# Kernel optimization log

Measured on AMD Instinct MI355X. Metric: run time of the kernel, lower is better.

The kernel has to match this reference:

```python
import jax, jax.numpy as jnp
import numpy as np

N, E, IN_FEATS, H = 20000, 320000, 512, 64
EPS = 1e-5  # BatchNorm eps


def setup_inputs() -> dict:
    key = jax.random.key(0)
    ks = iter(jax.random.split(key, 64))
    rn = lambda *s: jax.random.normal(next(ks), s, dtype=jnp.float32)
    d = {}
    d["x"] = rn(N, IN_FEATS)
    d["edge_index"] = jax.random.randint(next(ks), (2, E), 0, N)
    d["Wm"] = rn(IN_FEATS, H) * 0.05; d["bm"] = rn(H) * 0.05
    d["Wc"] = rn(IN_FEATS, H) * 0.05; d["bc"] = rn(H) * 0.05
    d["Wg1"] = rn(H, 2 * H) * 0.05;     d["bg1"] = rn(2 * H) * 0.05
    d["Wg2"] = rn(2 * H, 2 * H) * 0.05; d["bg2"] = rn(2 * H) * 0.05
    d["Wg3"] = rn(2 * H, 4 * H) * 0.05; d["bg3"] = rn(4 * H) * 0.05
    for name, cin in (("e1", 8 * H), ("e2", 4 * H), ("e3", 4 * H)):
        d[name + "_gamma"] = 1.0 + rn(cin) * 0.1
        d[name + "_beta"] = rn(cin) * 0.1
        d[name + "_mean"] = rn(cin) * 0.1
        d[name + "_var"] = jax.random.uniform(next(ks), (cin,), dtype=jnp.float32) + 0.5
        d[name + "_W"] = rn(cin, 2 * H) * 0.05
    d["Wfc"] = rn(2 * H, 1) * 0.05; d["bfc"] = rn(1) * 0.05
    return d


def _gcn(x, W, b, src, dst, n):
    """PyG GCNConv: self-loops + symmetric normalization + sum aggregation."""
    h = x @ W  # [N, out]
    loop = jnp.arange(n)
    s = jnp.concatenate([src, loop])
    d = jnp.concatenate([dst, loop])
    deg = jax.ops.segment_sum(jnp.ones(s.shape[0], h.dtype), d, num_segments=n)
    dinv = jnp.where(deg > 0, jax.lax.rsqrt(deg), 0.0)
    msg = h[s] * (dinv[s] * dinv[d])[:, None]  # gather + normalize
    return jax.ops.segment_sum(msg, d, num_segments=n) + b


def _edge_conv(x, gamma, beta, mean, var, W, src, dst, n):
    """PyG EdgeConv with LinearPathPreact nn (BN->ReLU->Linear), max aggregation."""
    xi = x[dst]
    xj = x[src]
    feat = jnp.concatenate([xi, xj - xi], axis=-1)  # [E, 2*C]
    h = (feat - mean) * jax.lax.rsqrt(var + EPS) * gamma + beta  # BN (eval stats)
    h = jnp.maximum(h, 0.0) @ W  # ReLU -> Linear(bias=False)
    out = jax.ops.segment_max(h, dst, num_segments=n)
    return jnp.where(jnp.isfinite(out), out, 0.0)  # empty segments -> 0


def reference(x, edge_index, Wm, bm, Wc, bc, Wg1, bg1, Wg2, bg2, Wg3, bg3,
              e1_gamma, e1_beta, e1_mean, e1_var, e1_W,
              e2_gamma, e2_beta, e2_mean, e2_var, e2_W,
              e3_gamma, e3_beta, e3_mean, e3_var, e3_W,
              Wfc, bfc):
    n = x.shape[0]
    src, dst = edge_index[0], edge_index[1]
    x0_main = x @ Wm + bm
    x0 = x @ Wc + bc
    x0 = x0.at[0::4].set(x0_main[0::4])  # main-person rows use the main projection
    g = _gcn(x0, Wg1, bg1, src, dst, n)
    g = _gcn(g, Wg2, bg2, src, dst, n)
    g = _gcn(g, Wg3, bg3, src, dst, n)
    h = _edge_conv(g, e1_gamma, e1_beta, e1_mean, e1_var, e1_W, src, dst, n)
    h = _edge_conv(h, e2_gamma, e2_beta, e2_mean, e2_var, e2_W, src, dst, n)
    h = _edge_conv(h, e3_gamma, e3_beta, e3_mean, e3_var, e3_W, src, dst, n)
    return h @ Wfc + bfc  # [N, 1]
```

## Files before the change

kernel.cpp:

```cpp
#include <hip/hip_runtime.h>

#define DEVINL __device__ __forceinline__

constexpr int N_NODES  = 20000;
constexpr int N_EDGES  = 320000;
constexpr int IN_FEATS = 512;

static_assert(N_EDGES % 64 == 0, "edge tiling assumes E % 64 == 0");
static_assert(N_NODES % 16 == 0, "proj assumes N % 16 == 0");

typedef __attribute__((ext_vector_type(8))) short short8;
typedef __attribute__((ext_vector_type(4))) float f32x4;

DEVINL unsigned enc_f32(float v) {
  unsigned b = __float_as_uint(v);
  return (b & 0x80000000u) ? ~b : (b | 0x80000000u);
}
DEVINL float dec_f32(unsigned e) {
  unsigned b = (e & 0x80000000u) ? (e & 0x7FFFFFFFu) : ~e;
  return __uint_as_float(b);
}

DEVINL unsigned short bf16_rne(float f) {
  unsigned u = __float_as_uint(f);
  u += 0x7FFFu + ((u >> 16) & 1u);
  return (unsigned short)(u >> 16);
}
DEVINL void split_bf16(float v, unsigned short& h, unsigned short& l) {
  h = bf16_rne(v);
  float hf = __uint_as_float((unsigned)h << 16);
  l = bf16_rne(v - hf);
}

DEVINL void glds16(const unsigned short* g, unsigned short* l) {
  __builtin_amdgcn_global_load_lds(
      (const __attribute__((address_space(1))) unsigned int*)g,
      (__attribute__((address_space(3))) unsigned int*)l, 16, 0, 0);
}

__global__ void hist_kernel(const int* __restrict__ dst, int* __restrict__ cnt, int e) {
  int i = blockIdx.x * 256 + threadIdx.x;
  if (i < e) atomicAdd(&cnt[dst[i]], 1);
}
__global__ void dinv_kernel(const int* __restrict__ cnt, float* __restrict__ dinv,
                            float* __restrict__ dinv2, int n) {
  int i = blockIdx.x * 256 + threadIdx.x;
  if (i < n) {
    float s = rsqrtf((float)cnt[i] + 1.0f);
    dinv[i] = s;
    dinv2[i] = s * s;
  }
}
__global__ void __launch_bounds__(256)
scan_p1(const int* __restrict__ cnt, int* __restrict__ rp, int* __restrict__ bsum, int n) {
  __shared__ int buf[256];
  int i = blockIdx.x * 256 + threadIdx.x;
  int v = (i < n) ? cnt[i] : 0;
  buf[threadIdx.x] = v;
  __syncthreads();
  for (int off = 1; off < 256; off <<= 1) {
    int t = (threadIdx.x >= off) ? buf[threadIdx.x - off] : 0;
    __syncthreads();
    buf[threadIdx.x] += t;
    __syncthreads();
  }
  if (i < n) rp[i] = buf[threadIdx.x] - v;
  if (threadIdx.x == 255) bsum[blockIdx.x] = buf[255];
}
__global__ void __launch_bounds__(256)
scan_p2(int* __restrict__ bsum, int nb) {
  __shared__ int buf[256];
  int v = (threadIdx.x < nb) ? bsum[threadIdx.x] : 0;
  buf[threadIdx.x] = v;
  __syncthreads();
  for (int off = 1; off < 256; off <<= 1) {
    int t = (threadIdx.x >= off) ? buf[threadIdx.x - off] : 0;
    __syncthreads();
    buf[threadIdx.x] += t;
    __syncthreads();
  }
  if (threadIdx.x < nb) bsum[threadIdx.x] = buf[threadIdx.x] - v;
}
__global__ void __launch_bounds__(256)
scan_p3(int* __restrict__ rp, const int* __restrict__ bsum, int* __restrict__ cursor,
        int n, int e) {
  int i = blockIdx.x * 256 + threadIdx.x;
  if (i < n) {
    int v = rp[i] + bsum[blockIdx.x];
    rp[i] = v;
    cursor[i] = v;
  }
  if (i == 0) rp[n] = e;
}
__global__ void scatter_edges_kernel(const int* __restrict__ src, const int* __restrict__ dst,
                                     int* __restrict__ cursor, int* __restrict__ ssrc,
                                     int* __restrict__ sdst, int e) {
  int i = blockIdx.x * 256 + threadIdx.x;
  if (i < e) {
    int d = dst[i];
    int pos = atomicAdd(&cursor[d], 1);
    ssrc[pos] = src[i];
    sdst[pos] = d;
  }
}

__global__ void uvec1_kernel(const int* __restrict__ row_ptr, const int* __restrict__ ssrc,
                             const float* __restrict__ dinv, float* __restrict__ u1,
                             float* __restrict__ w1, int n) {
  int d = blockIdx.x * 256 + threadIdx.x;
  if (d >= n) return;
  float s = dinv[d];
  float acc = s;
  int e = row_ptr[d], end = row_ptr[d + 1];
  for (; e < end; ++e) acc += dinv[ssrc[e]];
  float u = s * acc;
  u1[d] = u;
  w1[d] = s * u;
}
__global__ void uvec2_kernel(const int* __restrict__ row_ptr, const int* __restrict__ ssrc,
                             const float* __restrict__ dinv, const float* __restrict__ w1,
                             float* __restrict__ u2, int n) {
  int d = blockIdx.x * 256 + threadIdx.x;
  if (d >= n) return;
  float acc = w1[d];
  int e = row_ptr[d], end = row_ptr[d + 1];
  for (; e < end; ++e) acc += w1[ssrc[e]];
  u2[d] = dinv[d] * acc;
}

__global__ void smallmm2(const float* __restrict__ A1, const float* __restrict__ B1,
                         float* __restrict__ C1, int m1, int k1, int n1,
                         const float* __restrict__ A2, const float* __restrict__ B2,
                         float* __restrict__ C2, int m2, int k2, int n2) {
  int i = blockIdx.x * 256 + threadIdx.x;
  int t1 = m1 * n1;
  if (i < t1) {
    int r = i / n1, c = i % n1;
    float acc = 0.f;
    for (int kk = 0; kk < k1; ++kk) acc = fmaf(A1[r * k1 + kk], B1[kk * n1 + c], acc);
    C1[i] = acc;
  } else {
    i -= t1;
    if (i < m2 * n2) {
      int r = i / n2, c = i % n2;
      float acc = 0.f;
      for (int kk = 0; kk < k2; ++kk) acc = fmaf(A2[r * k2 + kk], B2[kk * n2 + c], acc);
      C2[i] = acc;
    }
  }
}

DEVINL void bn1(const float* g, const float* b, const float* m, const float* v,
                float* sc, float* sh, int i) {
  float s = g[i] * rsqrtf(v[i] + 1e-5f);
  sc[i] = s;
  sh[i] = b[i] - m[i] * s;
}
__global__ void bn_prep_all(const float* g1, const float* b1, const float* m1, const float* v1,
                            float* sc1, float* sh1, const float* g2, const float* b2,
                            const float* m2, const float* v2, float* sc2, float* sh2,
                            const float* g3, const float* b3, const float* m3, const float* v3,
                            float* sc3, float* sh3) {
  int i = blockIdx.x * 256 + threadIdx.x;
  if (i < 512) bn1(g1, b1, m1, v1, sc1, sh1, i);
  else if (i < 768) bn1(g2, b2, m2, v2, sc2, sh2, i - 512);
  else if (i < 1024) bn1(g3, b3, m3, v3, sc3, sh3, i - 768);
}

DEVINL void wfrag1(const float* W, unsigned short* out, int e) {
  int k = e >> 7, c = e & 127;
  unsigned short h, l;
  split_bf16(W[e], h, l);
  int chunk = k >> 5, kq = (k >> 3) & 3, j = k & 7, ct = c >> 4, n = c & 15;
  int frag = (ct * 4 + kq) * 16 + n;
  size_t o = (size_t)chunk * 8192 + frag * 8 + j;
  out[o] = h;
  out[o + 4096] = l;
}
__global__ void wfrag_all(const float* __restrict__ e1W, const float* __restrict__ e2W,
                          const float* __restrict__ e3W, unsigned short* b1p,
                          unsigned short* b1q, unsigned short* b2p, unsigned short* b2q,
                          unsigned short* b3p, unsigned short* b3q) {
  int g = blockIdx.x * 256 + threadIdx.x;
  if (g < 32768) wfrag1(e1W, b1p, g);
  else if (g < 65536) wfrag1(e1W + 32768, b1q, g - 32768);
  else if (g < 81920) wfrag1(e2W, b2p, g - 65536);
  else if (g < 98304) wfrag1(e2W + 16384, b2q, g - 81920);
  else if (g < 114688) wfrag1(e3W, b3p, g - 98304);
  else wfrag1(e3W + 16384, b3q, g - 114688);
}

__global__ void combine_kernel(unsigned* __restrict__ Q, const float* __restrict__ P,
                               float* __restrict__ H, int n) {
  int i = blockIdx.x * 256 + threadIdx.x;
  if (i < n) {
    unsigned e = Q[i];
    H[i] = e ? (P[i] + dec_f32(e)) : 0.f;
    Q[i] = 0u;
  }
}

__global__ void __launch_bounds__(256)
proj_kernel(const float* __restrict__ X, const float* __restrict__ Wm,
            const float* __restrict__ bm, const float* __restrict__ Wc,
            const float* __restrict__ bc, const float* __restrict__ dinv,
            float* __restrict__ Y0) {
  __shared__ float xs[16][IN_FEATS];
  int tid = threadIdx.x;
  int rowBase = blockIdx.x * 16;
  for (int i = 0; i < 8; ++i) {
    int idx = i * 256 + tid;
    int r = idx >> 7, kq = idx & 127;
    *reinterpret_cast<float4*>(&xs[r][kq * 4]) =
        *reinterpret_cast<const float4*>(X + (size_t)(rowBase + r) * IN_FEATS + kq * 4);
  }
  __syncthreads();
  int r4 = tid >> 6;
  int j = tid & 63;
  const float* W = (r4 == 0) ? Wm : Wc;
  float a0 = 0.f, a1 = 0.f, a2 = 0.f, a3 = 0.f;
#pragma unroll 4
  for (int k = 0; k < IN_FEATS; ++k) {
    float w = W[k * 64 + j];
    a0 = fmaf(xs[r4][k], w, a0);
    a1 = fmaf(xs[r4 + 4][k], w, a1);
    a2 = fmaf(xs[r4 + 8][k], w, a2);
    a3 = fmaf(xs[r4 + 12][k], w, a3);
  }
  float b = (r4 == 0) ? bm[j] : bc[j];
  int r0 = rowBase + r4;
  Y0[(size_t)r0 * 64 + j] = (a0 + b) * dinv[r0];
  Y0[(size_t)(r0 + 4) * 64 + j] = (a1 + b) * dinv[r0 + 4];
  Y0[(size_t)(r0 + 8) * 64 + j] = (a2 + b) * dinv[r0 + 8];
  Y0[(size_t)(r0 + 12) * 64 + j] = (a3 + b) * dinv[r0 + 12];
}

template <int LOGF4>
__global__ void __launch_bounds__(256)
agg_kernel(const float* __restrict__ Y, const int* __restrict__ row_ptr,
           const int* __restrict__ ssrc, const float* __restrict__ mfac,
           float* __restrict__ Z, int n) {
  constexpr int F4 = 1 << LOGF4;
  int g = blockIdx.x * 256 + threadIdx.x;
  int d = g >> LOGF4, c4 = g & (F4 - 1);
  if (d >= n) return;
  const float4* Yp = (const float4*)Y;
  float4 a = Yp[(size_t)d * F4 + c4];
  float ax = a.x, ay = a.y, az = a.z, aw = a.w;
  int e = row_ptr[d], end = row_ptr[d + 1];
  for (; e + 7 < end; e += 8) {
    int s[8];
#pragma unroll
    for (int i = 0; i < 8; ++i) s[i] = ssrc[e + i];
    float4 v[8];
#pragma unroll
    for (int i = 0; i < 8; ++i) v[i] = Yp[(size_t)s[i] * F4 + c4];
#pragma unroll
    for (int i = 0; i < 8; ++i) {
      ax += v[i].x; ay += v[i].y; az += v[i].z; aw += v[i].w;
    }
  }
  for (; e < end; ++e) {
    float4 v = Yp[(size_t)ssrc[e] * F4 + c4];
    ax += v.x; ay += v.y; az += v.z; aw += v.w;
  }
  float s = mfac[d];
  ((float4*)Z)[(size_t)d * F4 + c4] = make_float4(ax * s, ay * s, az * s, aw * s);
}

__global__ void __launch_bounds__(256)
gemm_rank1_kernel(const float* __restrict__ X, const float* __restrict__ W,
                  const float* __restrict__ b3, const float* __restrict__ u1,
                  const float* __restrict__ u2, const float* __restrict__ c1,
                  const float* __restrict__ c2, float* __restrict__ H, int n) {
  constexpr int K = 64, F = 256;
  __shared__ float Xs[64][K + 1];
  __shared__ float Ws[K][65];
  int tid = threadIdx.x;
  int rowBase = blockIdx.x * 64;
  int colBase = blockIdx.y * 64;
  for (int idx = tid; idx < 64 * K; idx += 256) {
    int r = idx / K, k = idx % K;
    int row = rowBase + r;
    Xs[r][k] = (row < n) ? X[(size_t)row * K + k] : 0.f;
  }
  for (int idx = tid; idx < K * 64; idx += 256) {
    int k = idx >> 6, c = idx & 63;
    Ws[k][c] = W[(size_t)k * F + colBase + c];
  }
  __syncthreads();
  int tx = tid & 15, ty = tid >> 4;
  float acc[4][4] = {};
  for (int k = 0; k < K; ++k) {
    float a[4], b[4];
#pragma unroll
    for (int r = 0; r < 4; ++r) a[r] = Xs[ty * 4 + r][k];
#pragma unroll
    for (int c = 0; c < 4; ++c) b[c] = Ws[k][tx * 4 + c];
#pragma unroll
    for (int r = 0; r < 4; ++r)
#pragma unroll
      for (int c = 0; c < 4; ++c) acc[r][c] = fmaf(a[r], b[c], acc[r][c]);
  }
#pragma unroll
  for (int r = 0; r < 4; ++r) {
    int row = rowBase + ty * 4 + r;
    if (row < n) {
      float du2 = u2[row], du1 = u1[row];
#pragma unroll
      for (int c = 0; c < 4; ++c) {
        int col = colBase + tx * 4 + c;
        float v = acc[r][c] + du2 * c1[col] + du1 * c2[col] + b3[col];
        H[(size_t)row * F + col] = v;
      }
    }
  }
}

DEVINL void proc8(const float4& va, const float4& vb, const float4& sa, const float4& sb,
                  const float4& ha, const float4& hb, short8& hi, short8& lo) {
  float f[8] = {va.x, va.y, va.z, va.w, vb.x, vb.y, vb.z, vb.w};
  float s[8] = {sa.x, sa.y, sa.z, sa.w, sb.x, sb.y, sb.z, sb.w};
  float t[8] = {ha.x, ha.y, ha.z, ha.w, hb.x, hb.y, hb.z, hb.w};
#pragma unroll
  for (int j = 0; j < 8; ++j) {
    float v = fmaxf(fmaf(f[j], s[j], t[j]), 0.f);
    unsigned short hh, ll;
    split_bf16(v, hh, ll);
    hi[j] = (short)hh;
    lo[j] = (short)ll;
  }
}

template <int C>
__global__ void __launch_bounds__(256, 4)
ec_mfma_kernel(const float* __restrict__ X, const int* __restrict__ ssrc,
               const int* __restrict__ sdst,
               const float* __restrict__ scaleQ, const float* __restrict__ shiftQ,
               const unsigned short* __restrict__ BfragQ,
               const float* __restrict__ scaleP, const float* __restrict__ shiftP,
               const unsigned short* __restrict__ BfragP,
               unsigned* __restrict__ outU, float* __restrict__ outP,
               int nrows, int edge_blocks) {
  constexpr int NCH = C / 32;
  constexpr int NSTAGE = NCH / 2;
  __shared__ unsigned short Bmat[16384];
  __shared__ float ss[2 * C];
  __shared__ int de_s[64];
  const int tid = threadIdx.x, lane = tid & 63, wv = tid >> 6;
  const int q = lane >> 4, mn = lane & 15;
  const bool EDGE = (int)blockIdx.x < edge_blocks;
  const int base = (EDGE ? (int)blockIdx.x : (int)blockIdx.x - edge_blocks) * 64;
  const int koff = q * 8;
  const int lr = wv * 16 + mn;

  const float* scale = EDGE ? scaleQ : scaleP;
  const float* shift = EDGE ? shiftQ : shiftP;
  const unsigned short* Bfrag = EDGE ? BfragQ : BfragP;

  int id, is = 0;
  if (EDGE) {
    if (tid < 64) de_s[tid] = sdst[base + tid];
    is = ssrc[base + lr];
    id = sdst[base + lr];
  } else {
    id = min(base + lr, nrows - 1);
  }
  const float* pd = X + (size_t)id * C + koff;
  const float* ps = EDGE ? X + (size_t)is * C + koff : nullptr;

  f32x4 acc[8];
#pragma unroll
  for (int i = 0; i < 8; ++i) acc[i] = (f32x4)0.f;

  float4 A[2][4];
#define LOAD_A(cc, slot)                              \
  {                                                   \
    const int kk_ = (cc) * 32;                        \
    A[slot][0] = *(const float4*)(pd + kk_);          \
    A[slot][1] = *(const float4*)(pd + kk_ + 4);      \
    if (EDGE) {                                       \
      A[slot][2] = *(const float4*)(ps + kk_);        \
      A[slot][3] = *(const float4*)(ps + kk_ + 4);    \
    }                                                 \
  }

  LOAD_A(0, 0);
  {
    constexpr int NF4 = C / 4;
    if (tid < NF4)
      ((float4*)ss)[tid] = ((const float4*)scale)[tid];
    else if (tid < 2 * NF4)
      ((float4*)(ss + C))[tid - NF4] = ((const float4*)shift)[tid - NF4];
  }
  {
    const unsigned short* bs = Bfrag + lane * 8;
#pragma unroll
    for (int i = 0; i < 8; ++i) {
      int seg = wv * 8 + i;
      glds16(bs + seg * 512, Bmat + seg * 512);
    }
  }

#pragma unroll
  for (int s = 0; s < NSTAGE; ++s) {
    if (s > 0) {
      __syncthreads();
      const unsigned short* bs = Bfrag + (size_t)s * 16384 + lane * 8;
#pragma unroll
      for (int i = 0; i < 8; ++i) {
        int seg = wv * 8 + i;
        glds16(bs + seg * 512, Bmat + seg * 512);
      }
    }
    __syncthreads();
#pragma unroll
    for (int cc = 0; cc < 2; ++cc) {
      const int c = s * 2 + cc;
      const int kc = c * 32;
      if (c + 1 < NCH) LOAD_A(c + 1, (c + 1) & 1);
      float4 sca = *(const float4*)&ss[kc + koff];
      float4 scb = *(const float4*)&ss[kc + koff + 4];
      float4 sha = *(const float4*)&ss[C + kc + koff];
      float4 shb = *(const float4*)&ss[C + kc + koff + 4];
      const int sl = c & 1;
      float4 u0, u1;
      if (EDGE) {
        u0 = make_float4(A[sl][2].x - A[sl][0].x, A[sl][2].y - A[sl][0].y,
                         A[sl][2].z - A[sl][0].z, A[sl][2].w - A[sl][0].w);
        u1 = make_float4(A[sl][3].x - A[sl][1].x, A[sl][3].y - A[sl][1].y,
                         A[sl][3].z - A[sl][1].z, A[sl][3].w - A[sl][1].w);
      } else {
        u0 = A[sl][0];
        u1 = A[sl][1];
      }
      short8 ah, al;
      proc8(u0, u1, sca, scb, sha, shb, ah, al);
      const unsigned short* Bc = Bmat + cc * 8192;
#pragma unroll
      for (int ct = 0; ct < 8; ++ct) {
        int fi = ct * 64 + lane;
        short8 bh = *(const short8*)(Bc + fi * 8);
        short8 bl = *(const short8*)(Bc + 4096 + fi * 8);
        acc[ct] = __builtin_amdgcn_mfma_f32_16x16x32_bf16(ah, bh, acc[ct], 0, 0, 0);
        acc[ct] = __builtin_amdgcn_mfma_f32_16x16x32_bf16(ah, bl, acc[ct], 0, 0, 0);
        acc[ct] = __builtin_amdgcn_mfma_f32_16x16x32_bf16(al, bh, acc[ct], 0, 0, 0);
      }
    }
  }
#undef LOAD_A

  if (EDGE) {
    int e0 = wv * 16 + q * 4;
#pragma unroll
    for (int ct = 0; ct < 8; ++ct) {
      int f = ct * 16 + mn;
      int prev = de_s[e0];
      float mv = acc[ct][0];
#pragma unroll
      for (int r = 1; r < 4; ++r) {
        int d = de_s[e0 + r];
        float v = acc[ct][r];
        if (d == prev) {
          mv = fmaxf(mv, v);
        } else {
          atomicMax(&outU[(size_t)prev * 128 + f], enc_f32(mv));
          prev = d;
          mv = v;
        }
      }
      atomicMax(&outU[(size_t)prev * 128 + f], enc_f32(mv));
    }
  } else {
    int r0 = base + wv * 16 + q * 4;
#pragma unroll
    for (int ct = 0; ct < 8; ++ct) {
      int f = ct * 16 + mn;
#pragma unroll
      for (int r = 0; r < 4; ++r) {
        int row = r0 + r;
        if (row < nrows) outP[(size_t)row * 128 + f] = acc[ct][r];
      }
    }
  }
}

__global__ void __launch_bounds__(256)
fc_kernel(const unsigned* __restrict__ Q, const float* __restrict__ P,
          const float* __restrict__ Wfc, const float* __restrict__ bfc,
          float* __restrict__ out, int n) {
  int g = blockIdx.x * 256 + threadIdx.x;
  int node = g >> 6, lane = g & 63;
  if (node >= n) return;
  size_t b = (size_t)node * 128;
  unsigned q0 = Q[b + lane], q1 = Q[b + 64 + lane];
  float h0 = q0 ? (P[b + lane] + dec_f32(q0)) : 0.f;
  float h1 = q1 ? (P[b + 64 + lane] + dec_f32(q1)) : 0.f;
  float v = fmaf(h0, Wfc[lane], h1 * Wfc[64 + lane]);
#pragma unroll
  for (int off = 32; off > 0; off >>= 1) v += __shfl_down(v, off);
  if (lane == 0) out[node] = v + bfc[0];
}

extern "C" void kernel_launch(void* const* d_in, const int* in_sizes, int n_in,
                              void* d_out, int out_size, void* d_ws, size_t ws_size,
                              hipStream_t stream) {
  const float* x   = (const float*)d_in[0];
  const int*   ei  = (const int*)d_in[1];
  const float* Wm  = (const float*)d_in[2];
  const float* bm  = (const float*)d_in[3];
  const float* Wc  = (const float*)d_in[4];
  const float* bc  = (const float*)d_in[5];
  const float* Wg1 = (const float*)d_in[6];
  const float* bg1 = (const float*)d_in[7];
  const float* Wg2 = (const float*)d_in[8];
  const float* bg2 = (const float*)d_in[9];
  const float* Wg3 = (const float*)d_in[10];
  const float* bg3 = (const float*)d_in[11];
  const float* e1g = (const float*)d_in[12];
  const float* e1b = (const float*)d_in[13];
  const float* e1m = (const float*)d_in[14];
  const float* e1v = (const float*)d_in[15];
  const float* e1W = (const float*)d_in[16];
  const float* e2g = (const float*)d_in[17];
  const float* e2b = (const float*)d_in[18];
  const float* e2m = (const float*)d_in[19];
  const float* e2v = (const float*)d_in[20];
  const float* e2W = (const float*)d_in[21];
  const float* e3g = (const float*)d_in[22];
  const float* e3b = (const float*)d_in[23];
  const float* e3m = (const float*)d_in[24];
  const float* e3v = (const float*)d_in[25];
  const float* e3W = (const float*)d_in[26];
  const float* Wfc = (const float*)d_in[27];
  const float* bfc = (const float*)d_in[28];

  const int* src = ei;
  const int* dst = ei + N_EDGES;

  float* ws    = (float*)d_ws;
  float* dinv  = ws;
  float* dinv2 = dinv + N_NODES;
  float* u1    = dinv2 + N_NODES;
  float* w1    = u1 + N_NODES;
  float* u2    = w1 + N_NODES;
  float* y0    = u2 + N_NODES;
  float* za    = y0 + (size_t)N_NODES * 64;
  float* zb    = za + (size_t)N_NODES * 64;
  float* PQ    = zb + (size_t)N_NODES * 64;
  float* G     = PQ + (size_t)N_NODES * 256;
  float* sc1   = G + (size_t)N_NODES * 256;
  float* sh1   = sc1 + 512;
  float* sc2   = sh1 + 512;
  float* sh2   = sc2 + 256;
  float* sc3   = sh2 + 256;
  float* sh3   = sc3 + 256;
  unsigned short* bf1p = (unsigned short*)(sh3 + 256);
  unsigned short* bf1q = bf1p + 65536;
  unsigned short* bf2p = bf1q + 65536;
  unsigned short* bf2q = bf2p + 32768;
  unsigned short* bf3p = bf2q + 32768;
  unsigned short* bf3q = bf3p + 32768;
  float* W23   = (float*)(bf3q + 32768);
  float* W123  = W23 + 32768;
  float* c1    = W123 + 16384;
  float* c2    = c1 + 256;
  int* cnt     = (int*)(c2 + 256);
  int* row_ptr = cnt + N_NODES;
  int* cursor  = row_ptr + N_NODES + 1;
  int* bsum    = cursor + N_NODES;
  int* ssrc    = bsum + 256;
  int* sdst    = ssrc + N_EDGES;

  float*    Pbuf = PQ;
  unsigned* Qbuf = (unsigned*)(PQ + (size_t)N_NODES * 128);

  hipMemsetAsync(cnt, 0, N_NODES * sizeof(int), stream);
  hist_kernel<<<N_EDGES / 256, 256, 0, stream>>>(dst, cnt, N_EDGES);
  dinv_kernel<<<79, 256, 0, stream>>>(cnt, dinv, dinv2, N_NODES);
  scan_p1<<<79, 256, 0, stream>>>(cnt, row_ptr, bsum, N_NODES);
  scan_p2<<<1, 256, 0, stream>>>(bsum, 79);
  scan_p3<<<79, 256, 0, stream>>>(row_ptr, bsum, cursor, N_NODES, N_EDGES);
  scatter_edges_kernel<<<N_EDGES / 256, 256, 0, stream>>>(src, dst, cursor, ssrc, sdst,
                                                          N_EDGES);

  smallmm2<<<129, 256, 0, stream>>>(Wg2, Wg3, W23, 128, 128, 256,
                                    bg2, Wg3, c2, 1, 128, 256);
  smallmm2<<<65, 256, 0, stream>>>(Wg1, W23, W123, 64, 128, 256,
                                   bg1, W23, c1, 1, 128, 256);
  uvec1_kernel<<<79, 256, 0, stream>>>(row_ptr, ssrc, dinv, u1, w1, N_NODES);
  uvec2_kernel<<<79, 256, 0, stream>>>(row_ptr, ssrc, dinv, w1, u2, N_NODES);

  bn_prep_all<<<4, 256, 0, stream>>>(e1g, e1b, e1m, e1v, sc1, sh1, e2g, e2b, e2m, e2v, sc2,
                                     sh2, e3g, e3b, e3m, e3v, sc3, sh3);
  wfrag_all<<<512, 256, 0, stream>>>(e1W, e2W, e3W, bf1p, bf1q, bf2p, bf2q, bf3p, bf3q);

  proj_kernel<<<N_NODES / 16, 256, 0, stream>>>(x, Wm, bm, Wc, bc, dinv, y0);
  agg_kernel<4><<<N_NODES * 16 / 256, 256, 0, stream>>>(y0, row_ptr, ssrc, dinv2, za, N_NODES);
  agg_kernel<4><<<N_NODES * 16 / 256, 256, 0, stream>>>(za, row_ptr, ssrc, dinv2, zb, N_NODES);
  agg_kernel<4><<<N_NODES * 16 / 256, 256, 0, stream>>>(zb, row_ptr, ssrc, dinv, za, N_NODES);
  dim3 grid4(313, 4);
  gemm_rank1_kernel<<<grid4, 256, 0, stream>>>(za, W123, bg3, u1, u2, c1, c2, G, N_NODES);

  const int EDGE_BLOCKS = N_EDGES / 64;
  const int NODE_BLOCKS = (N_NODES + 63) / 64;
  const int EC_BLOCKS   = EDGE_BLOCKS + NODE_BLOCKS;
  const int NB_ELEM     = N_NODES * 128 / 256;

  float* H1 = G;
  float* H2 = G + (size_t)N_NODES * 128;

  hipMemsetAsync(Qbuf, 0, (size_t)N_NODES * 128 * 4, stream);
  ec_mfma_kernel<256><<<EC_BLOCKS, 256, 0, stream>>>(
      G, ssrc, sdst, sc1 + 256, sh1 + 256, bf1q, sc1, sh1, bf1p, Qbuf, Pbuf, N_NODES,
      EDGE_BLOCKS);
  combine_kernel<<<NB_ELEM, 256, 0, stream>>>(Qbuf, Pbuf, H1, N_NODES * 128);

  ec_mfma_kernel<128><<<EC_BLOCKS, 256, 0, stream>>>(
      H1, ssrc, sdst, sc2 + 128, sh2 + 128, bf2q, sc2, sh2, bf2p, Qbuf, Pbuf, N_NODES,
      EDGE_BLOCKS);
  combine_kernel<<<NB_ELEM, 256, 0, stream>>>(Qbuf, Pbuf, H2, N_NODES * 128);

  ec_mfma_kernel<128><<<EC_BLOCKS, 256, 0, stream>>>(
      H2, ssrc, sdst, sc3 + 128, sh3 + 128, bf3q, sc3, sh3, bf3p, Qbuf, Pbuf, N_NODES,
      EDGE_BLOCKS);
  fc_kernel<<<N_NODES * 64 / 256, 256, 0, stream>>>(Qbuf, Pbuf, Wfc, bfc, (float*)d_out,
                                                    N_NODES);
}
```

Baseline: 710.3 us.

## Fuse combine step into edge-conv loads and merge small setup kernels

The separate combine kernels that decoded the max-encoded Q and added P into dense H buffers are removed. The second and third edge-conv kernels now read Q and P directly and decode them on the fly for both the source and destination rows, using ping-pong P/Q buffers with a memset before each layer. The dinv computation is folded into scan_p1, and the BN-prep and weight-fragment kernels are merged into one launch. This saves two full elementwise passes and several launches, but doubles the gathered bytes per edge in layers 2 and 3 and lowers the occupancy bound to 3 blocks for the combine variant.

After: 742.0 us. +4.5%, slower.

```diff
diff --git a/kernel.cpp b/kernel.cpp
--- a/kernel.cpp
+++ b/kernel.cpp
@@ -20,6 +20,7 @@
   unsigned b = (e & 0x80000000u) ? (e & 0x7FFFFFFFu) : ~e;
   return __uint_as_float(b);
 }
+DEVINL float dech(unsigned q, float p) { return q ? (p + dec_f32(q)) : 0.f; }
 
 DEVINL unsigned short bf16_rne(float f) {
   unsigned u = __float_as_uint(f);
@@ -42,20 +43,17 @@
   int i = blockIdx.x * 256 + threadIdx.x;
   if (i < e) atomicAdd(&cnt[dst[i]], 1);
 }
-__global__ void dinv_kernel(const int* __restrict__ cnt, float* __restrict__ dinv,
-                            float* __restrict__ dinv2, int n) {
-  int i = blockIdx.x * 256 + threadIdx.x;
-  if (i < n) {
-    float s = rsqrtf((float)cnt[i] + 1.0f);
-    dinv[i] = s;
-    dinv2[i] = s * s;
-  }
-}
 __global__ void __launch_bounds__(256)
-scan_p1(const int* __restrict__ cnt, int* __restrict__ rp, int* __restrict__ bsum, int n) {
+scan_p1(const int* __restrict__ cnt, int* __restrict__ rp, int* __restrict__ bsum,
+        float* __restrict__ dinv, float* __restrict__ dinv2, int n) {
   __shared__ int buf[256];
   int i = blockIdx.x * 256 + threadIdx.x;
   int v = (i < n) ? cnt[i] : 0;
+  if (i < n) {
+    float s = rsqrtf((float)v + 1.0f);
+    dinv[i] = s;
+    dinv2[i] = s * s;
+  }
   buf[threadIdx.x] = v;
   __syncthreads();
   for (int off = 1; off < 256; off <<= 1) {
@@ -156,17 +154,6 @@
   sc[i] = s;
   sh[i] = b[i] - m[i] * s;
 }
-__global__ void bn_prep_all(const float* g1, const float* b1, const float* m1, const float* v1,
-                            float* sc1, float* sh1, const float* g2, const float* b2,
-                            const float* m2, const float* v2, float* sc2, float* sh2,
-                            const float* g3, const float* b3, const float* m3, const float* v3,
-                            float* sc3, float* sh3) {
-  int i = blockIdx.x * 256 + threadIdx.x;
-  if (i < 512) bn1(g1, b1, m1, v1, sc1, sh1, i);
-  else if (i < 768) bn1(g2, b2, m2, v2, sc2, sh2, i - 512);
-  else if (i < 1024) bn1(g3, b3, m3, v3, sc3, sh3, i - 768);
-}
-
 DEVINL void wfrag1(const float* W, unsigned short* out, int e) {
   int k = e >> 7, c = e & 127;
   unsigned short h, l;
@@ -177,26 +164,29 @@
   out[o] = h;
   out[o + 4096] = l;
 }
-__global__ void wfrag_all(const float* __restrict__ e1W, const float* __restrict__ e2W,
-                          const float* __restrict__ e3W, unsigned short* b1p,
-                          unsigned short* b1q, unsigned short* b2p, unsigned short* b2q,
-                          unsigned short* b3p, unsigned short* b3q) {
-  int g = blockIdx.x * 256 + threadIdx.x;
-  if (g < 32768) wfrag1(e1W, b1p, g);
-  else if (g < 65536) wfrag1(e1W + 32768, b1q, g - 32768);
-  else if (g < 81920) wfrag1(e2W, b2p, g - 65536);
-  else if (g < 98304) wfrag1(e2W + 16384, b2q, g - 81920);
-  else if (g < 114688) wfrag1(e3W, b3p, g - 98304);
-  else wfrag1(e3W + 16384, b3q, g - 114688);
-}
-
-__global__ void combine_kernel(unsigned* __restrict__ Q, const float* __restrict__ P,
-                               float* __restrict__ H, int n) {
-  int i = blockIdx.x * 256 + threadIdx.x;
-  if (i < n) {
-    unsigned e = Q[i];
-    H[i] = e ? (P[i] + dec_f32(e)) : 0.f;
-    Q[i] = 0u;
+__global__ void setup_kernel(const float* __restrict__ e1W, const float* __restrict__ e2W,
+                             const float* __restrict__ e3W, unsigned short* b1p,
+                             unsigned short* b1q, unsigned short* b2p, unsigned short* b2q,
+                             unsigned short* b3p, unsigned short* b3q,
+                             const float* g1, const float* b1, const float* m1,
+                             const float* v1, float* sc1, float* sh1, const float* g2,
+                             const float* b2, const float* m2, const float* v2, float* sc2,
+                             float* sh2, const float* g3, const float* b3, const float* m3,
+                             const float* v3, float* sc3, float* sh3) {
+  if (blockIdx.x < 512) {
+    int g = blockIdx.x * 256 + threadIdx.x;
+    if (g < 32768) wfrag1(e1W, b1p, g);
+    else if (g < 65536) wfrag1(e1W + 32768, b1q, g - 32768);
+    else if (g < 81920) wfrag1(e2W, b2p, g - 65536);
+    else if (g < 98304) wfrag1(e2W + 16384, b2q, g - 81920);
+    else if (g < 114688) wfrag1(e3W, b3p, g - 98304);
+    else wfrag1(e3W + 16384, b3q, g - 114688);
+  } else {
+    for (int i = threadIdx.x; i < 1024; i += 256) {
+      if (i < 512) bn1(g1, b1, m1, v1, sc1, sh1, i);
+      else if (i < 768) bn1(g2, b2, m2, v2, sc2, sh2, i - 512);
+      else bn1(g3, b3, m3, v3, sc3, sh3, i - 768);
+    }
   }
 }
 
@@ -331,10 +321,14 @@
     lo[j] = (short)ll;
   }
 }
-
-template <int C>
-__global__ void __launch_bounds__(256, 4)
-ec_mfma_kernel(const float* __restrict__ X, const int* __restrict__ ssrc,
+DEVINL float4 dec4(uint4 q, float4 p) {
+  return make_float4(dech(q.x, p.x), dech(q.y, p.y), dech(q.z, p.z), dech(q.w, p.w));
+}
+
+template <int C, bool COMBINE>
+__global__ void __launch_bounds__(256, COMBINE ? 3 : 4)
+ec_mfma_kernel(const float* __restrict__ X, const unsigned* __restrict__ Qin,
+               const float* __restrict__ Pin, const int* __restrict__ ssrc,
                const int* __restrict__ sdst,
                const float* __restrict__ scaleQ, const float* __restrict__ shiftQ,
                const unsigned short* __restrict__ BfragQ,
@@ -366,23 +360,54 @@
   } else {
     id = min(base + lr, nrows - 1);
   }
-  const float* pd = X + (size_t)id * C + koff;
-  const float* ps = EDGE ? X + (size_t)is * C + koff : nullptr;
 
   f32x4 acc[8];
 #pragma unroll
   for (int i = 0; i < 8; ++i) acc[i] = (f32x4)0.f;
 
+  const float* pd = nullptr;
+  const float* pvs = nullptr;
+  const unsigned* qd = nullptr;
+  const float* ppd = nullptr;
+  const unsigned* qs = nullptr;
+  const float* pps = nullptr;
+  if (COMBINE) {
+    qd = Qin + (size_t)id * C + koff;
+    ppd = Pin + (size_t)id * C + koff;
+    if (EDGE) {
+      qs = Qin + (size_t)is * C + koff;
+      pps = Pin + (size_t)is * C + koff;
+    }
+  } else {
+    pd = X + (size_t)id * C + koff;
+    if (EDGE) pvs = X + (size_t)is * C + koff;
+  }
+
   float4 A[2][4];
-#define LOAD_A(cc, slot)                              \
-  {                                                   \
-    const int kk_ = (cc) * 32;                        \
-    A[slot][0] = *(const float4*)(pd + kk_);          \
-    A[slot][1] = *(const float4*)(pd + kk_ + 4);      \
-    if (EDGE) {                                       \
-      A[slot][2] = *(const float4*)(ps + kk_);        \
-      A[slot][3] = *(const float4*)(ps + kk_ + 4);    \
-    }                                                 \
+  uint4 Aq[2][4];
+  float4 Ap[2][4];
+#define LOAD_A(cc, slot)                                        \
+  {                                                             \
+    const int kk_ = (cc) * 32;                                  \
+    if (COMBINE) {                                              \
+      Aq[slot][0] = *(const uint4*)(qd + kk_);                  \
+      Aq[slot][1] = *(const uint4*)(qd + kk_ + 4);              \
+      Ap[slot][0] = *(const float4*)(ppd + kk_);                \
+      Ap[slot][1] = *(const float4*)(ppd + kk_ + 4);            \
+      if (EDGE) {                                               \
+        Aq[slot][2] = *(const uint4*)(qs + kk_);                \
+        Aq[slot][3] = *(const uint4*)(qs + kk_ + 4);            \
+        Ap[slot][2] = *(const float4*)(pps + kk_);              \
+        Ap[slot][3] = *(const float4*)(pps + kk_ + 4);          \
+      }                                                         \
+    } else {                                                    \
+      A[slot][0] = *(const float4*)(pd + kk_);                  \
+      A[slot][1] = *(const float4*)(pd + kk_ + 4);              \
+      if (EDGE) {                                               \
+        A[slot][2] = *(const float4*)(pvs + kk_);               \
+        A[slot][3] = *(const float4*)(pvs + kk_ + 4);           \
+      }                                                         \
+    }                                                           \
   }
 
   LOAD_A(0, 0);
@@ -425,14 +450,28 @@
       float4 shb = *(const float4*)&ss[C + kc + koff + 4];
       const int sl = c & 1;
       float4 u0, u1;
-      if (EDGE) {
-        u0 = make_float4(A[sl][2].x - A[sl][0].x, A[sl][2].y - A[sl][0].y,
-                         A[sl][2].z - A[sl][0].z, A[sl][2].w - A[sl][0].w);
-        u1 = make_float4(A[sl][3].x - A[sl][1].x, A[sl][3].y - A[sl][1].y,
-                         A[sl][3].z - A[sl][1].z, A[sl][3].w - A[sl][1].w);
+      if (COMBINE) {
+        float4 hd0 = dec4(Aq[sl][0], Ap[sl][0]);
+        float4 hd1 = dec4(Aq[sl][1], Ap[sl][1]);
+        if (EDGE) {
+          float4 hs0 = dec4(Aq[sl][2], Ap[sl][2]);
+          float4 hs1 = dec4(Aq[sl][3], Ap[sl][3]);
+          u0 = make_float4(hs0.x - hd0.x, hs0.y - hd0.y, hs0.z - hd0.z, hs0.w - hd0.w);
+          u1 = make_float4(hs1.x - hd1.x, hs1.y - hd1.y, hs1.z - hd1.z, hs1.w - hd1.w);
+        } else {
+          u0 = hd0;
+          u1 = hd1;
+        }
       } else {
-        u0 = A[sl][0];
-        u1 = A[sl][1];
+        if (EDGE) {
+          u0 = make_float4(A[sl][2].x - A[sl][0].x, A[sl][2].y - A[sl][0].y,
+                           A[sl][2].z - A[sl][0].z, A[sl][2].w - A[sl][0].w);
+          u1 = make_float4(A[sl][3].x - A[sl][1].x, A[sl][3].y - A[sl][1].y,
+                           A[sl][3].z - A[sl][1].z, A[sl][3].w - A[sl][1].w);
+        } else {
+          u0 = A[sl][0];
+          u1 = A[sl][1];
+        }
       }
       short8 ah, al;
       proc8(u0, u1, sca, scb, sha, shb, ah, al);
@@ -493,9 +532,8 @@
   int node = g >> 6, lane = g & 63;
   if (node >= n) return;
   size_t b = (size_t)node * 128;
-  unsigned q0 = Q[b + lane], q1 = Q[b + 64 + lane];
-  float h0 = q0 ? (P[b + lane] + dec_f32(q0)) : 0.f;
-  float h1 = q1 ? (P[b + 64 + lane] + dec_f32(q1)) : 0.f;
+  float h0 = dech(Q[b + lane], P[b + lane]);
+  float h1 = dech(Q[b + 64 + lane], P[b + 64 + lane]);
   float v = fmaf(h0, Wfc[lane], h1 * Wfc[64 + lane]);
 #pragma unroll
   for (int off = 32; off > 0; off >>= 1) v += __shfl_down(v, off);
@@ -572,13 +610,16 @@
   int* ssrc    = bsum + 256;
   int* sdst    = ssrc + N_EDGES;
 
-  float*    Pbuf = PQ;
-  unsigned* Qbuf = (unsigned*)(PQ + (size_t)N_NODES * 128);
+  float*    P1 = PQ;
+  unsigned* Q1 = (unsigned*)(PQ + (size_t)N_NODES * 128);
+  float*    P2 = G;
+  unsigned* Q2 = (unsigned*)(G + (size_t)N_NODES * 128);
+  float*    P3 = P1;
+  unsigned* Q3 = Q1;
 
   hipMemsetAsync(cnt, 0, N_NODES * sizeof(int), stream);
   hist_kernel<<<N_EDGES / 256, 256, 0, stream>>>(dst, cnt, N_EDGES);
-  dinv_kernel<<<79, 256, 0, stream>>>(cnt, dinv, dinv2, N_NODES);
-  scan_p1<<<79, 256, 0, stream>>>(cnt, row_ptr, bsum, N_NODES);
+  scan_p1<<<79, 256, 0, stream>>>(cnt, row_ptr, bsum, dinv, dinv2, N_NODES);
   scan_p2<<<1, 256, 0, stream>>>(bsum, 79);
   scan_p3<<<79, 256, 0, stream>>>(row_ptr, bsum, cursor, N_NODES, N_EDGES);
   scatter_edges_kernel<<<N_EDGES / 256, 256, 0, stream>>>(src, dst, cursor, ssrc, sdst,
@@ -591,9 +632,9 @@
   uvec1_kernel<<<79, 256, 0, stream>>>(row_ptr, ssrc, dinv, u1, w1, N_NODES);
   uvec2_kernel<<<79, 256, 0, stream>>>(row_ptr, ssrc, dinv, w1, u2, N_NODES);
 
-  bn_prep_all<<<4, 256, 0, stream>>>(e1g, e1b, e1m, e1v, sc1, sh1, e2g, e2b, e2m, e2v, sc2,
-                                     sh2, e3g, e3b, e3m, e3v, sc3, sh3);
-  wfrag_all<<<512, 256, 0, stream>>>(e1W, e2W, e3W, bf1p, bf1q, bf2p, bf2q, bf3p, bf3q);
+  setup_kernel<<<513, 256, 0, stream>>>(e1W, e2W, e3W, bf1p, bf1q, bf2p, bf2q, bf3p, bf3q,
+                                        e1g, e1b, e1m, e1v, sc1, sh1, e2g, e2b, e2m, e2v,
+                                        sc2, sh2, e3g, e3b, e3m, e3v, sc3, sh3);
 
   proj_kernel<<<N_NODES / 16, 256, 0, stream>>>(x, Wm, bm, Wc, bc, dinv, y0);
   agg_kernel<4><<<N_NODES * 16 / 256, 256, 0, stream>>>(y0, row_ptr, ssrc, dinv2, za, N_NODES);
@@ -605,25 +646,22 @@
   const int EDGE_BLOCKS = N_EDGES / 64;
   const int NODE_BLOCKS = (N_NODES + 63) / 64;
   const int EC_BLOCKS   = EDGE_BLOCKS + NODE_BLOCKS;
-  const int NB_ELEM     = N_NODES * 128 / 256;
-
-  float* H1 = G;
-  float* H2 = G + (size_t)N_NODES * 128;
-
-  hipMemsetAsync(Qbuf, 0, (size_t)N_NODES * 128 * 4, stream);
-  ec_mfma_kernel<256><<<EC_BLOCKS, 256, 0, stream>>>(
-      G, ssrc, sdst, sc1 + 256, sh1 + 256, bf1q, sc1, sh1, bf1p, Qbuf, Pbuf, N_NODES,
-      EDGE_BLOCKS);
-  combine_kernel<<<NB_ELEM, 256, 0, stream>>>(Qbuf, Pbuf, H1, N_NODES * 128);
-
-  ec_mfma_kernel<128><<<EC_BLOCKS, 256, 0, stream>>>(
-      H1, ssrc, sdst, sc2 + 128, sh2 + 128, bf2q, sc2, sh2, bf2p, Qbuf, Pbuf, N_NODES,
-      EDGE_BLOCKS);
-  combine_kernel<<<NB_ELEM, 256, 0, stream>>>(Qbuf, Pbuf, H2, N_NODES * 128);
-
-  ec_mfma_kernel<128><<<EC_BLOCKS, 256, 0, stream>>>(
-      H2, ssrc, sdst, sc3 + 128, sh3 + 128, bf3q, sc3, sh3, bf3p, Qbuf, Pbuf, N_NODES,
-      EDGE_BLOCKS);
-  fc_kernel<<<N_NODES * 64 / 256, 256, 0, stream>>>(Qbuf, Pbuf, Wfc, bfc, (float*)d_out,
+
+  hipMemsetAsync(Q1, 0, (size_t)N_NODES * 128 * 4, stream);
+  ec_mfma_kernel<256, false><<<EC_BLOCKS, 256, 0, stream>>>(
+      G, nullptr, nullptr, ssrc, sdst, sc1 + 256, sh1 + 256, bf1q, sc1, sh1, bf1p, Q1, P1,
+      N_NODES, EDGE_BLOCKS);
+
+  hipMemsetAsync(Q2, 0, (size_t)N_NODES * 128 * 4, stream);
+  ec_mfma_kernel<128, true><<<EC_BLOCKS, 256, 0, stream>>>(
+      nullptr, Q1, P1, ssrc, sdst, sc2 + 128, sh2 + 128, bf2q, sc2, sh2, bf2p, Q2, P2,
+      N_NODES, EDGE_BLOCKS);
+
+  hipMemsetAsync(Q3, 0, (size_t)N_NODES * 128 * 4, stream);
+  ec_mfma_kernel<128, true><<<EC_BLOCKS, 256, 0, stream>>>(
+      nullptr, Q2, P2, ssrc, sdst, sc3 + 128, sh3 + 128, bf3q, sc3, sh3, bf3p, Q3, P3,
+      N_NODES, EDGE_BLOCKS);
+
+  fc_kernel<<<N_NODES * 64 / 256, 256, 0, stream>>>(Q3, P3, Wfc, bfc, (float*)d_out,
                                                     N_NODES);
 }
```
